# Optimization experiments

Hardware: AMD Instinct MI355X
Metric: run time of the kernel (lower is better)

## Reference

```python
import math
import jax, jax.numpy as jnp
import numpy as np

NEG_INF_FILL = 1e-09  # faithful to the source: masked positions get +1e-09, not -inf

B, H, S, D = 2, 16, 2048, 64


def setup_inputs() -> dict:
    key = jax.random.key(0)
    kq, kk, kv = jax.random.split(key, 3)
    q = jax.random.normal(kq, (B, H, S, D), dtype=jnp.float32)
    k = jax.random.normal(kk, (B, H, S, D), dtype=jnp.float32)
    v = jax.random.normal(kv, (B, H, S, D), dtype=jnp.float32)
    # causal boolean mask, broadcast over heads: [B, 1, S, S]
    causal = jnp.tril(jnp.ones((S, S), dtype=bool))
    attention_mask = jnp.broadcast_to(causal[None, None, :, :], (B, 1, S, S))
    return {"q": q, "k": k, "v": v, "attention_mask": attention_mask}


def reference(q, k, v, attention_mask):
    d_k = q.shape[-1]
    # scores: [B, H, S, S]
    scores = jnp.einsum("bhqd,bhkd->bhqk", q, k) / math.sqrt(d_k)
    scores = jnp.where(attention_mask, scores, NEG_INF_FILL)
    attn = jax.nn.softmax(scores, axis=-1)
    # output: [B, H, S, D]
    return jnp.einsum("bhqk,bhkd->bhqd", attn, v)
```

## Files before the change

kernel.cpp:

```cpp
#include <hip/hip_runtime.h>
#include <hip/hip_bf16.h>


#define SEQ 2048
#define DIM 64
#define KS_STRIDE 72
#define PS_STRIDE 72
#define QSCALE 0.18033688011112042f

typedef _Float16 half_t;
typedef _Float16 half8  __attribute__((ext_vector_type(8)));
typedef _Float16 half4v __attribute__((ext_vector_type(4)));
typedef _Float16 half2v __attribute__((ext_vector_type(2)));
typedef float    float4v __attribute__((ext_vector_type(4)));

__global__ __launch_bounds__(256, 2)
void attn_mfma_kernel(const float* __restrict__ Q,
                      const float* __restrict__ K,
                      const float* __restrict__ V,
                      float* __restrict__ O) {
    __shared__ half_t smem_h[64 * KS_STRIDE + 64 * KS_STRIDE + 4 * 32 * PS_STRIDE];
    half_t* Ks  = smem_h;
    half_t* VTs = smem_h + 64 * KS_STRIDE;
    half_t* Ps  = smem_h + 2 * 64 * KS_STRIDE;

    const int tid = threadIdx.x;
    const int l   = tid & 63;
    const int w   = tid >> 6;
    const int lx  = l & 15;
    const int h   = l >> 4;
    const int bh  = blockIdx.x;
    const int qb  = 15 - (int)blockIdx.y;
    const int qbase = qb * 128;
    const int nkt = 2 * qb + 2;
    const int n_tail = SEQ - nkt * 64;

    const float* Qh = Q + (size_t)bh * SEQ * DIM;
    const float* Kh = K + (size_t)bh * SEQ * DIM;
    const float* Vh = V + (size_t)bh * SEQ * DIM;
    float*       Oh = O + (size_t)bh * SEQ * DIM;

    half8 qf[2][2];
    const int qrow_w = qbase + 32 * w;
    #pragma unroll
    for (int nt = 0; nt < 2; ++nt) {
        const float* qp = Qh + (size_t)(qrow_w + 16 * nt + lx) * DIM;
        #pragma unroll
        for (int s = 0; s < 2; ++s) {
            float4v a = *(const float4v*)(qp + 32 * s + 8 * h);
            float4v b = *(const float4v*)(qp + 32 * s + 8 * h + 4);
            half8 f;
            f[0] = (half_t)(a[0] * QSCALE); f[1] = (half_t)(a[1] * QSCALE);
            f[2] = (half_t)(a[2] * QSCALE); f[3] = (half_t)(a[3] * QSCALE);
            f[4] = (half_t)(b[0] * QSCALE); f[5] = (half_t)(b[1] * QSCALE);
            f[6] = (half_t)(b[2] * QSCALE); f[7] = (half_t)(b[3] * QSCALE);
            qf[nt][s] = f;
        }
    }

    float4v acc[4][2];
    #pragma unroll
    for (int mt = 0; mt < 4; ++mt)
        #pragma unroll
        for (int nt = 0; nt < 2; ++nt) acc[mt][nt] = (float4v){0.f, 0.f, 0.f, 0.f};
    float lp[2] = {0.f, 0.f};

    const int c = tid & 15;
    const int r0 = tid >> 4;

    float4v kreg[4], vreg[4];
    {
        #pragma unroll
        for (int u = 0; u < 4; ++u)
            kreg[u] = *(const float4v*)(Kh + (r0 + 16 * u) * DIM + 4 * c);
        #pragma unroll
        for (int u = 0; u < 2; ++u) {
            const float* vp = Vh + (size_t)(2 * (r0 + 16 * u)) * DIM + 4 * c;
            vreg[2 * u]     = *(const float4v*)(vp);
            vreg[2 * u + 1] = *(const float4v*)(vp + DIM);
        }
    }

    for (int kt = 0; kt < nkt; ++kt) {
        __syncthreads();

        #pragma unroll
        for (int u = 0; u < 4; ++u) {
            int kr = r0 + 16 * u;
            half4v hk;
            hk[0] = (half_t)kreg[u][0]; hk[1] = (half_t)kreg[u][1];
            hk[2] = (half_t)kreg[u][2]; hk[3] = (half_t)kreg[u][3];
            *(half4v*)(Ks + kr * KS_STRIDE + 4 * c) = hk;
        }
        #pragma unroll
        for (int u = 0; u < 2; ++u) {
            int kp = r0 + 16 * u;
            #pragma unroll
            for (int i = 0; i < 4; ++i) {
                int ir = (i + c + (c >> 2)) & 3;
                int dr = 4 * c + ir;
                half2v hv;
                hv[0] = (half_t)vreg[2 * u][ir];
                hv[1] = (half_t)vreg[2 * u + 1][ir];
                *(half2v*)(VTs + dr * KS_STRIDE + 2 * kp) = hv;
            }
        }
        __syncthreads();

        if (kt + 1 < nkt) {
            const float* Kt = Kh + (size_t)(kt + 1) * 64 * DIM;
            const float* Vt = Vh + (size_t)(kt + 1) * 64 * DIM;
            #pragma unroll
            for (int u = 0; u < 4; ++u)
                kreg[u] = *(const float4v*)(Kt + (r0 + 16 * u) * DIM + 4 * c);
            #pragma unroll
            for (int u = 0; u < 2; ++u) {
                const float* vp = Vt + (size_t)(2 * (r0 + 16 * u)) * DIM + 4 * c;
                vreg[2 * u]     = *(const float4v*)(vp);
                vreg[2 * u + 1] = *(const float4v*)(vp + DIM);
            }
        }

        const int key_base = kt * 64;
        #pragma unroll
        for (int mt = 0; mt < 4; ++mt) {
            half8 ak0 = *(const half8*)(Ks + (16 * mt + lx) * KS_STRIDE + 8 * h);
            half8 ak1 = *(const half8*)(Ks + (16 * mt + lx) * KS_STRIDE + 32 + 8 * h);
            const bool need_mask = (key_base + 16 * mt + 15) > qrow_w;
            #pragma unroll
            for (int nt = 0; nt < 2; ++nt) {
                float4v ct = (float4v){0.f, 0.f, 0.f, 0.f};
                ct = __builtin_amdgcn_mfma_f32_16x16x32_f16(ak0, qf[nt][0], ct, 0, 0, 0);
                ct = __builtin_amdgcn_mfma_f32_16x16x32_f16(ak1, qf[nt][1], ct, 0, 0, 0);
                float p[4];
                #pragma unroll
                for (int r = 0; r < 4; ++r)
                    p[r] = __builtin_amdgcn_exp2f(ct[r]);
                if (need_mask) {
                    const int qg = qrow_w + 16 * nt + lx;
                    const int kb = key_base + 16 * mt + 4 * h;
                    #pragma unroll
                    for (int r = 0; r < 4; ++r)
                        if (kb + r > qg) p[r] = 1.0f;
                }
                lp[nt] += (p[0] + p[1]) + (p[2] + p[3]);
                half4v hp;
                hp[0] = (half_t)p[0]; hp[1] = (half_t)p[1];
                hp[2] = (half_t)p[2]; hp[3] = (half_t)p[3];
                *(half4v*)(Ps + w * (32 * PS_STRIDE) + (16 * nt + lx) * PS_STRIDE
                           + 16 * mt + 4 * h) = hp;
            }
        }

        half8 pf[2][2];
        #pragma unroll
        for (int nt = 0; nt < 2; ++nt)
            #pragma unroll
            for (int s = 0; s < 2; ++s)
                pf[nt][s] = *(const half8*)(Ps + w * (32 * PS_STRIDE)
                                            + (16 * nt + lx) * PS_STRIDE + 32 * s + 8 * h);
        #pragma unroll
        for (int mt = 0; mt < 4; ++mt) {
            half8 av0 = *(const half8*)(VTs + (16 * mt + lx) * KS_STRIDE + 8 * h);
            half8 av1 = *(const half8*)(VTs + (16 * mt + lx) * KS_STRIDE + 32 + 8 * h);
            #pragma unroll
            for (int nt = 0; nt < 2; ++nt) {
                float4v ct = acc[mt][nt];
                ct = __builtin_amdgcn_mfma_f32_16x16x32_f16(av0, pf[nt][0], ct, 0, 0, 0);
                ct = __builtin_amdgcn_mfma_f32_16x16x32_f16(av1, pf[nt][1], ct, 0, 0, 0);
                acc[mt][nt] = ct;
            }
        }
    }

    float linv[2];
    #pragma unroll
    for (int nt = 0; nt < 2; ++nt) {
        float s = lp[nt];
        s += __shfl_xor(s, 16, 64);
        s += __shfl_xor(s, 32, 64);
        linv[nt] = 1.0f / (s + (float)n_tail);
    }

    float ts0 = 0.f, ts1 = 0.f, ts2 = 0.f, ts3 = 0.f;
    {
        const int tstart = nkt * 64;
        const float* vp = Vh + (size_t)tstart * DIM + 4 * c;
        #pragma unroll 4
        for (int k = tstart + r0; k < SEQ; k += 16) {
            float4v x = *(const float4v*)(Vh + (size_t)k * DIM + 4 * c);
            ts0 += x[0]; ts1 += x[1]; ts2 += x[2]; ts3 += x[3];
        }
        (void)vp;
    }
    __syncthreads();
    float* preS = (float*)smem_h;
    float* vtf  = ((float*)smem_h) + 8320;
    {
        float4v pv = {ts0, ts1, ts2, ts3};
        *(float4v*)(preS + r0 * 68 + 4 * c) = pv;
    }
    __syncthreads();
    if (tid < 64) {
        float s = 0.f;
        #pragma unroll
        for (int p = 0; p < 16; ++p) s += preS[p * 68 + tid];
        vtf[tid] = s;
    }
    __syncthreads();
    float vt_l[4][4];
    #pragma unroll
    for (int mt = 0; mt < 4; ++mt)
        #pragma unroll
        for (int r = 0; r < 4; ++r) vt_l[mt][r] = vtf[16 * mt + 4 * h + r];

    float* Osm = (float*)smem_h;
    #pragma unroll
    for (int mt = 0; mt < 4; ++mt)
        #pragma unroll
        for (int nt = 0; nt < 2; ++nt)
            #pragma unroll
            for (int r = 0; r < 4; ++r) {
                float o = (acc[mt][nt][r] + vt_l[mt][r]) * linv[nt];
                Osm[w * (32 * 65) + (16 * nt + lx) * 65 + 16 * mt + 4 * h + r] = o;
            }
    __syncthreads();
    #pragma unroll
    for (int u = 0; u < 8; ++u) {
        int row = r0 + 16 * u;
        int dc = 4 * c;
        const float* src = Osm + (row >> 5) * (32 * 65) + (row & 31) * 65 + dc;
        float4v ov = {src[0], src[1], src[2], src[3]};
        *(float4v*)(Oh + (size_t)(qbase + row) * DIM + dc) = ov;
    }
}

extern "C" void kernel_launch(void* const* d_in, const int* in_sizes, int n_in,
                              void* d_out, int out_size, void* d_ws, size_t ws_size,
                              hipStream_t stream) {
    const float* q = (const float*)d_in[0];
    const float* k = (const float*)d_in[1];
    const float* v = (const float*)d_in[2];
    float* out = (float*)d_out;
    attn_mfma_kernel<<<dim3(32, 16), 256, 0, stream>>>(q, k, v, out);
}
```

Before: 148.7 us.

## Double-buffer K/V tiles in LDS and keep P in registers via 16x16x16 MFMA

Staging of K and V^T now goes into two alternating LDS buffers, so the next tile is written after the PV step. This removes one of the two barriers per key tile, and the global loads run two tiles ahead. The probability tile no longer round-trips through LDS: the QK^T accumulator layout is fed straight into 16x16x16 f16 MFMAs as the B operand. The trade is twice as many, smaller MFMAs and more live registers for the extra K/V prefetch, which risks spills under launch bounds of 2 blocks.

Result: slower. 195.6 us (+31.6%).

```diff
diff --git a/kernel.cpp b/kernel.cpp
--- a/kernel.cpp
+++ b/kernel.cpp
@@ -5,7 +5,6 @@
 #define SEQ 2048
 #define DIM 64
 #define KS_STRIDE 72
-#define PS_STRIDE 72
 #define QSCALE 0.18033688011112042f
 
 typedef _Float16 half_t;
@@ -19,10 +18,7 @@
                       const float* __restrict__ K,
                       const float* __restrict__ V,
                       float* __restrict__ O) {
-    __shared__ half_t smem_h[64 * KS_STRIDE + 64 * KS_STRIDE + 4 * 32 * PS_STRIDE];
-    half_t* Ks  = smem_h;
-    half_t* VTs = smem_h + 64 * KS_STRIDE;
-    half_t* Ps  = smem_h + 2 * 64 * KS_STRIDE;
+    __shared__ half_t smem_h[2 * 2 * 64 * KS_STRIDE];
 
     const int tid = threadIdx.x;
     const int l   = tid & 63;
@@ -65,32 +61,32 @@
         for (int nt = 0; nt < 2; ++nt) acc[mt][nt] = (float4v){0.f, 0.f, 0.f, 0.f};
     float lp[2] = {0.f, 0.f};
 
-    const int c = tid & 15;
+    const int c  = tid & 15;
     const int r0 = tid >> 4;
 
     float4v kreg[4], vreg[4];
-    {
+    auto load_tile = [&](int kt) {
+        const float* Kt = Kh + (size_t)kt * 64 * DIM;
+        const float* Vt = Vh + (size_t)kt * 64 * DIM;
         #pragma unroll
         for (int u = 0; u < 4; ++u)
-            kreg[u] = *(const float4v*)(Kh + (r0 + 16 * u) * DIM + 4 * c);
+            kreg[u] = *(const float4v*)(Kt + (r0 + 16 * u) * DIM + 4 * c);
         #pragma unroll
         for (int u = 0; u < 2; ++u) {
-            const float* vp = Vh + (size_t)(2 * (r0 + 16 * u)) * DIM + 4 * c;
+            const float* vp = Vt + (size_t)(2 * (r0 + 16 * u)) * DIM + 4 * c;
             vreg[2 * u]     = *(const float4v*)(vp);
             vreg[2 * u + 1] = *(const float4v*)(vp + DIM);
         }
-    }
-
-    for (int kt = 0; kt < nkt; ++kt) {
-        __syncthreads();
-
+    };
+    auto stage = [&](half_t* dstK) {
+        half_t* dstV = dstK + 64 * KS_STRIDE;
         #pragma unroll
         for (int u = 0; u < 4; ++u) {
             int kr = r0 + 16 * u;
             half4v hk;
             hk[0] = (half_t)kreg[u][0]; hk[1] = (half_t)kreg[u][1];
             hk[2] = (half_t)kreg[u][2]; hk[3] = (half_t)kreg[u][3];
-            *(half4v*)(Ks + kr * KS_STRIDE + 4 * c) = hk;
+            *(half4v*)(dstK + kr * KS_STRIDE + 4 * c) = hk;
         }
         #pragma unroll
         for (int u = 0; u < 2; ++u) {
@@ -102,26 +98,22 @@
                 half2v hv;
                 hv[0] = (half_t)vreg[2 * u][ir];
                 hv[1] = (half_t)vreg[2 * u + 1][ir];
-                *(half2v*)(VTs + dr * KS_STRIDE + 2 * kp) = hv;
-            }
-        }
+                *(half2v*)(dstV + dr * KS_STRIDE + 2 * kp) = hv;
+            }
+        }
+    };
+
+    load_tile(0);
+    stage(smem_h);
+    load_tile(1);
+
+    for (int kt = 0; kt < nkt; ++kt) {
         __syncthreads();
-
-        if (kt + 1 < nkt) {
-            const float* Kt = Kh + (size_t)(kt + 1) * 64 * DIM;
-            const float* Vt = Vh + (size_t)(kt + 1) * 64 * DIM;
-            #pragma unroll
-            for (int u = 0; u < 4; ++u)
-                kreg[u] = *(const float4v*)(Kt + (r0 + 16 * u) * DIM + 4 * c);
-            #pragma unroll
-            for (int u = 0; u < 2; ++u) {
-                const float* vp = Vt + (size_t)(2 * (r0 + 16 * u)) * DIM + 4 * c;
-                vreg[2 * u]     = *(const float4v*)(vp);
-                vreg[2 * u + 1] = *(const float4v*)(vp + DIM);
-            }
-        }
+        const half_t* Ks  = smem_h + (kt & 1) * (2 * 64 * KS_STRIDE);
+        const half_t* VTs = Ks + 64 * KS_STRIDE;
 
         const int key_base = kt * 64;
+        half4v pf[2][4];
         #pragma unroll
         for (int mt = 0; mt < 4; ++mt) {
             half8 ak0 = *(const half8*)(Ks + (16 * mt + lx) * KS_STRIDE + 8 * h);
@@ -147,29 +139,29 @@
                 half4v hp;
                 hp[0] = (half_t)p[0]; hp[1] = (half_t)p[1];
                 hp[2] = (half_t)p[2]; hp[3] = (half_t)p[3];
-                *(half4v*)(Ps + w * (32 * PS_STRIDE) + (16 * nt + lx) * PS_STRIDE
-                           + 16 * mt + 4 * h) = hp;
-            }
-        }
-
-        half8 pf[2][2];
-        #pragma unroll
-        for (int nt = 0; nt < 2; ++nt)
-            #pragma unroll
-            for (int s = 0; s < 2; ++s)
-                pf[nt][s] = *(const half8*)(Ps + w * (32 * PS_STRIDE)
-                                            + (16 * nt + lx) * PS_STRIDE + 32 * s + 8 * h);
-        #pragma unroll
-        for (int mt = 0; mt < 4; ++mt) {
-            half8 av0 = *(const half8*)(VTs + (16 * mt + lx) * KS_STRIDE + 8 * h);
-            half8 av1 = *(const half8*)(VTs + (16 * mt + lx) * KS_STRIDE + 32 + 8 * h);
+                pf[nt][mt] = hp;
+            }
+        }
+
+        #pragma unroll
+        for (int mtd = 0; mtd < 4; ++mtd) {
+            half4v av[4];
+            #pragma unroll
+            for (int s = 0; s < 4; ++s)
+                av[s] = *(const half4v*)(VTs + (16 * mtd + lx) * KS_STRIDE + 16 * s + 4 * h);
             #pragma unroll
             for (int nt = 0; nt < 2; ++nt) {
-                float4v ct = acc[mt][nt];
-                ct = __builtin_amdgcn_mfma_f32_16x16x32_f16(av0, pf[nt][0], ct, 0, 0, 0);
-                ct = __builtin_amdgcn_mfma_f32_16x16x32_f16(av1, pf[nt][1], ct, 0, 0, 0);
-                acc[mt][nt] = ct;
-            }
+                float4v ct = acc[mtd][nt];
+                #pragma unroll
+                for (int s = 0; s < 4; ++s)
+                    ct = __builtin_amdgcn_mfma_f32_16x16x16f16(av[s], pf[nt][s], ct, 0, 0, 0);
+                acc[mtd][nt] = ct;
+            }
+        }
+
+        if (kt + 1 < nkt) {
+            stage(smem_h + ((kt + 1) & 1) * (2 * 64 * KS_STRIDE));
+            if (kt + 2 < nkt) load_tile(kt + 2);
         }
     }
 
@@ -185,13 +177,11 @@
     float ts0 = 0.f, ts1 = 0.f, ts2 = 0.f, ts3 = 0.f;
     {
         const int tstart = nkt * 64;
-        const float* vp = Vh + (size_t)tstart * DIM + 4 * c;
         #pragma unroll 4
         for (int k = tstart + r0; k < SEQ; k += 16) {
             float4v x = *(const float4v*)(Vh + (size_t)k * DIM + 4 * c);
             ts0 += x[0]; ts1 += x[1]; ts2 += x[2]; ts3 += x[3];
         }
-        (void)vp;
     }
     __syncthreads();
     float* preS = (float*)smem_h;
```
